# Kernel optimization log

Hardware: AMD Instinct MI355X
Metric: run time of the kernel (lower is better)

## Reference

```python
import jax, jax.numpy as jnp
import numpy as np

B, C, N, K = 32, 1024, 2048, 64


def fps_indices(x, num):
    """Farthest-feature sampling. x: (B, N, C). Returns int32 indices (B, num).
    Deterministic start at index 0 (standard PointNet++ style loop)."""
    b, n, _ = x.shape

    def step(carry, _):
        dists, farthest = carry
        centroid = jnp.take_along_axis(x, farthest[:, None, None], axis=1)  # (B,1,C)
        d = jnp.sum((x - centroid) ** 2, axis=-1)  # (B,N)
        dists = jnp.minimum(dists, d)
        nxt = jnp.argmax(dists, axis=1).astype(jnp.int32)
        return (dists, nxt), farthest

    init = (jnp.full((b, n), 1e10, x.dtype), jnp.zeros((b,), jnp.int32))
    _, idx = jax.lax.scan(step, init, None, length=num)
    return idx.T  # (B, num)


def conv1x1(w, bias, x):
    # w: (out,in), x: (B,in,n) -> (B,out,n)
    return jnp.einsum('oi,bin->bon', w, x) + bias[:, None]


def setup_inputs() -> dict:
    key = jax.random.key(0)
    ks = jax.random.split(key, 16)
    s = 0.02
    return {
        'point_feat': jax.random.normal(ks[0], (B, C, N), jnp.float32),
        'global_feat': jax.random.normal(ks[1], (B, C), jnp.float32),
        'ps1_w': jax.random.normal(ks[2], (C, 128, K), jnp.float32) * s,
        'ps1_b': jnp.zeros((128,), jnp.float32),
        'm1c1_w': jax.random.normal(ks[3], (128, 2 * C + 128), jnp.float32) * s,
        'm1c1_b': jnp.zeros((128,), jnp.float32),
        'm1c2_w': jax.random.normal(ks[4], (128, 128), jnp.float32) * s,
        'm1c2_b': jnp.zeros((128,), jnp.float32),
        'm1sc_w': jax.random.normal(ks[5], (128, 2 * C + 128), jnp.float32) * s,
        'm1sc_b': jnp.zeros((128,), jnp.float32),
        'm2c1_w': jax.random.normal(ks[6], (64, 128), jnp.float32) * s,
        'm2c1_b': jnp.zeros((64,), jnp.float32),
        'm2c2_w': jax.random.normal(ks[7], (3, 64), jnp.float32) * s,
        'm2c2_b': jnp.zeros((3,), jnp.float32),
    }


def reference(point_feat, global_feat, ps1_w, ps1_b, m1c1_w, m1c1_b,
              m1c2_w, m1c2_b, m1sc_w, m1sc_b, m2c1_w, m2c1_b, m2c2_w, m2c2_b):
    # ffs: farthest-feature sample + gather
    xt = jnp.transpose(point_feat, (0, 2, 1))            # (B,N,C)
    idx = fps_indices(xt, K)                             # (B,K)
    feat_ffs = jnp.take_along_axis(xt, idx[:, :, None], axis=1)  # (B,K,C)
    feat_ffs = jnp.transpose(feat_ffs, (0, 2, 1))        # (B,C,K)

    # ConvTranspose1d on a length-1 input == outer product with kernel
    x1 = jnp.einsum('bi,iok->bok', global_feat, ps1_w) + ps1_b[:, None]  # (B,128,K)

    gf = jnp.broadcast_to(global_feat[:, :, None], (B, C, K))
    cat = jnp.concatenate([x1, feat_ffs, gf], axis=1)    # (B,2176,K)

    # MLP_Res
    shortcut = conv1x1(m1sc_w, m1sc_b, cat)
    h = conv1x1(m1c2_w, m1c2_b, jax.nn.relu(conv1x1(m1c1_w, m1c1_b, cat))) + shortcut

    # mlp_2
    pred = conv1x1(m2c2_w, m2c2_b, jax.nn.relu(conv1x1(m2c1_w, m2c1_b, h)))  # (B,3,K)
    return jnp.transpose(pred, (0, 2, 1))                # (B,K,3)
```

## Files before the change

### kernel.cpp

```cpp
#include <hip/hip_runtime.h>

#define BB_ 32
#define CC_ 1024
#define NN_ 2048
#define KK_ 64

typedef __bf16 bf16x8 __attribute__((ext_vector_type(8)));
typedef __bf16 bf16x2 __attribute__((ext_vector_type(2)));
typedef float f32x4 __attribute__((ext_vector_type(4)));
typedef unsigned int u32;

__device__ inline unsigned short f2bf_rn(float f) {
    unsigned u = __float_as_uint(f);
    unsigned r = (u + 0x7fffu + ((u >> 16) & 1u)) >> 16;
    return (unsigned short)r;
}

__device__ inline unsigned pack_bf16_rn(float f0, float f1) {
#if __has_builtin(__builtin_amdgcn_cvt_pk_bf16_f32)
    union { bf16x2 v; unsigned u; } x;
    x.v = __builtin_amdgcn_cvt_pk_bf16_f32(f0, f1);
    return x.u;
#else
    return (unsigned)f2bf_rn(f0) | ((unsigned)f2bf_rn(f1) << 16);
#endif
}

__device__ inline void gload16(const void* g, void* l) {
    __builtin_amdgcn_global_load_lds(
        (const __attribute__((address_space(1))) u32*)g,
        (__attribute__((address_space(3))) u32*)l, 16, 0, 0);
}

__device__ void convert_body(const float* __restrict__ X,
                             unsigned char* __restrict__ Xc, int g0,
                             int cid, int t) {
    int chunk = cid & 7;
    int kt = (cid >> 3) & 31;
    int lb = cid >> 8;
    int n = chunk * 256 + t;
    int b = g0 + lb;
    const float* Xb = X + (size_t)b * CC_ * NN_;
    unsigned char* dst = Xc + (((size_t)lb * 32 + kt) * NN_ + n) * 128;
    int sw = n & 7;
#pragma unroll
    for (int q = 0; q < 4; q++) {
        float f[8];
#pragma unroll
        for (int j = 0; j < 8; j++)
            f[j] = Xb[(size_t)(kt * 32 + q * 8 + j) * NN_ + n];
        union { unsigned u[4]; uint4 v; } hq, lq;
#pragma unroll
        for (int j2 = 0; j2 < 4; j2++) {
            float a = f[2 * j2], c = f[2 * j2 + 1];
            unsigned hp = pack_bf16_rn(a, c);
            float h0f = __uint_as_float((hp & 0xffffu) << 16);
            float h1f = __uint_as_float(hp & 0xffff0000u);
            hq.u[j2] = hp;
            lq.u[j2] = pack_bf16_rn(a - h0f, c - h1f);
        }
        int p = q ^ sw;
        *(uint4*)(dst + (p << 4)) = hq.v;
        *(uint4*)(dst + ((p ^ 4) << 4)) = lq.v;
    }
}

__global__ void convert_kernel(const float* __restrict__ X,
                               unsigned char* __restrict__ Xc, int g0) {
    convert_body(X, Xc, g0, blockIdx.x, threadIdx.x);
}

__device__ void fps_block(const float* Gb, int* idx, int b) {
    __shared__ float swv[2][4];
    __shared__ int swi[2][4];
    int t = threadIdx.x;
    float dist[8], nr[8];
#pragma unroll
    for (int r = 0; r < 8; r++) {
        nr[r] = Gb[(size_t)(t + 256 * r) * (NN_ + 1)];
        dist[r] = 1e10f;
    }
    if (t == 0) idx[b * KK_] = 0;
    int far = 0;
    for (int k = 1; k < KK_; k++) {
        float nf = Gb[(size_t)far * (NN_ + 1)];
        const float* grow = Gb + (size_t)far * NN_;
        float v = -1.f;
        int pi = 0;
#pragma unroll
        for (int r = 0; r < 8; r++) {
            float d = nr[r] + nf - 2.f * grow[t + 256 * r];
            dist[r] = fminf(dist[r], d);
            if (dist[r] > v) { v = dist[r]; pi = t + 256 * r; }
        }
#pragma unroll
        for (int off = 32; off; off >>= 1) {
            float ov = __shfl_down(v, off);
            int oi = __shfl_down(pi, off);
            if (ov > v || (ov == v && oi < pi)) { v = ov; pi = oi; }
        }
        int par = k & 1;
        if ((t & 63) == 0) { swv[par][t >> 6] = v; swi[par][t >> 6] = pi; }
        __syncthreads();
        float bv = swv[par][0];
        int bi = swi[par][0];
#pragma unroll
        for (int ww = 1; ww < 4; ww++) {
            float wv2 = swv[par][ww]; int wi2 = swi[par][ww];
            if (wv2 > bv || (wv2 == bv && wi2 < bi)) { bv = wv2; bi = wi2; }
        }
        far = bi;
        if (t == 0) idx[b * KK_ + k] = bi;
    }
}

__global__ __launch_bounds__(256, 3) void gram_fps_kernel(
    const unsigned char* __restrict__ Xc, float* __restrict__ G,
    const float* Gprev, int* __restrict__ idx, int nFps, int g0prev,
    const float* __restrict__ X, unsigned char* __restrict__ XcNext,
    int g0next, int nGram, int gs) {
    int bx = (int)blockIdx.x;
    if (bx < nFps) {
        fps_block(Gprev + (size_t)bx * NN_ * NN_, idx, g0prev + bx);
        return;
    }
    bx -= nFps;
    if (bx >= nGram) {
        convert_body(X, XcNext, g0next, bx - nGram, threadIdx.x);
        return;
    }
    int lb = bx % gs;
    int tt = bx / gs;
    int tn = (int)((sqrtf(8.f * tt + 1.f) - 1.f) * 0.5f);
    while ((tn + 1) * (tn + 2) / 2 <= tt) tn++;
    while (tn * (tn + 1) / 2 > tt) tn--;
    int tm = tt - tn * (tn + 1) / 2;
    bool diag = (tm == tn);
    int t = threadIdx.x;
    __shared__ __align__(16) unsigned char sA[16384];
    __shared__ __align__(16) unsigned char sB[16384];

    const unsigned char* XcB = Xc + (size_t)lb * 32 * NN_ * 128;
    int w = t >> 6, l = t & 63;
    int m0w = (w & 1) * 64, n0w = (w >> 1) * 64;
    int q = l >> 4, rr = l & 15;

    f32x4 zero = {0.f, 0.f, 0.f, 0.f};
    f32x4 acc[4][4];
#pragma unroll
    for (int mt = 0; mt < 4; mt++)
#pragma unroll
        for (int nt = 0; nt < 4; nt++) acc[mt][nt] = zero;

    const unsigned char* sBp = diag ? sA : sB;
    for (int kt = 0; kt < 32; kt++) {
        const unsigned char* Ab = XcB + ((size_t)kt * NN_ + (size_t)tm * 128) * 128;
        const unsigned char* Bb = XcB + ((size_t)kt * NN_ + (size_t)tn * 128) * 128;
        __syncthreads();
#pragma unroll
        for (int r = 0; r < 4; r++)
            gload16(Ab + r * 4096 + t * 16, sA + r * 4096 + t * 16);
        if (!diag) {
#pragma unroll
            for (int r = 0; r < 4; r++)
                gload16(Bb + r * 4096 + t * 16, sB + r * 4096 + t * 16);
        }
        __syncthreads();

        bf16x8 ah[4], al[4], bh[4], bl[4];
#pragma unroll
        for (int mt = 0; mt < 4; mt++) {
            int ra = m0w + mt * 16 + rr;
            int pa = q ^ (ra & 7);
            ah[mt] = *(const bf16x8*)(sA + ra * 128 + (pa << 4));
            al[mt] = *(const bf16x8*)(sA + ra * 128 + ((pa ^ 4) << 4));
            int rb = n0w + mt * 16 + rr;
            int pb = q ^ (rb & 7);
            bh[mt] = *(const bf16x8*)(sBp + rb * 128 + (pb << 4));
            bl[mt] = *(const bf16x8*)(sBp + rb * 128 + ((pb ^ 4) << 4));
        }
#pragma unroll
        for (int mt = 0; mt < 4; mt++)
#pragma unroll
            for (int nt = 0; nt < 4; nt++) {
                acc[mt][nt] = __builtin_amdgcn_mfma_f32_16x16x32_bf16(ah[mt], bh[nt], acc[mt][nt], 0, 0, 0);
                acc[mt][nt] = __builtin_amdgcn_mfma_f32_16x16x32_bf16(ah[mt], bl[nt], acc[mt][nt], 0, 0, 0);
                acc[mt][nt] = __builtin_amdgcn_mfma_f32_16x16x32_bf16(al[mt], bh[nt], acc[mt][nt], 0, 0, 0);
            }
    }

    float* Gb = G + (size_t)lb * NN_ * NN_;
    int i0 = tm * 128, j0 = tn * 128;
    int cc = l & 15;
#pragma unroll
    for (int mt = 0; mt < 4; mt++)
#pragma unroll
        for (int nt = 0; nt < 4; nt++)
#pragma unroll
            for (int r = 0; r < 4; r++) {
                int gi = i0 + m0w + mt * 16 + q * 4 + r;
                int gj = j0 + n0w + nt * 16 + cc;
                float val = acc[mt][nt][r];
                Gb[(size_t)gi * NN_ + gj] = val;
                if (!diag) Gb[(size_t)gj * NN_ + gi] = val;
            }
}

__global__ void x1_fps_kernel(const float* __restrict__ gf, const float* __restrict__ w,
                              const float* __restrict__ bias, float* __restrict__ cat,
                              const float* Gprev, int* __restrict__ idx,
                              int g0prev, int nFps) {
    if ((int)blockIdx.x < nFps) {
        fps_block(Gprev + (size_t)blockIdx.x * NN_ * NN_, idx, g0prev + blockIdx.x);
        return;
    }
    int bid = blockIdx.x - nFps;
    int t = threadIdx.x;
    int okg = bid & 31, bg = bid >> 5;
    int ok = okg * 256 + t;
    int o = ok >> 6, k = ok & 63;
    float acc[8];
#pragma unroll
    for (int j = 0; j < 8; j++) acc[j] = 0.f;
    const float* g = gf + (size_t)(bg * 8) * CC_;
    for (int i = 0; i < CC_; i++) {
        float wv = w[(size_t)(i * 128 + o) * KK_ + k];
#pragma unroll
        for (int j = 0; j < 8; j++) acc[j] += g[j * CC_ + i] * wv;
    }
    float bv = bias[o];
#pragma unroll
    for (int j = 0; j < 8; j++)
        cat[((size_t)(bg * 8 + j) * 2176 + o) * KK_ + k] = acc[j] + bv;
}

__global__ void catfill_kernel(const float* __restrict__ X, const float* __restrict__ gf,
                               const int* __restrict__ idx, float* __restrict__ cat) {
    int b = blockIdx.y;
    int t = threadIdx.x;
    int ch = 128 + blockIdx.x * 4 + (t >> 6);
    int k = t & 63;
    float v;
    if (ch < 1152) {
        int c = ch - 128;
        int ik = idx[b * KK_ + k];
        v = X[((size_t)b * CC_ + c) * NN_ + ik];
    } else {
        v = gf[b * CC_ + (ch - 1152)];
    }
    cat[((size_t)b * 2176 + ch) * KK_ + k] = v;
}

__global__ void mlp1_kernel(const float* __restrict__ cat, const float* __restrict__ w1,
                            const float* __restrict__ b1, const float* __restrict__ wsc,
                            const float* __restrict__ bsc, float* __restrict__ t1,
                            float* __restrict__ sc) {
    __shared__ float red[2][16][64];
    int b = blockIdx.y, og = blockIdx.x;
    int t = threadIdx.x;
    int k = t & 63, sub = t >> 6;
    int o0 = og * 4;
    const float* cb = cat + (size_t)b * 2176 * KK_;
    float a1[4], a2[4];
#pragma unroll
    for (int j = 0; j < 4; j++) { a1[j] = 0.f; a2[j] = 0.f; }
    int iBeg = sub * 544;
    int off = (b & 7) * 68;
#pragma unroll 1
    for (int seg = 0; seg < 2; seg++) {
        int s0 = iBeg + (seg ? 0 : off);
        int s1 = seg ? iBeg + off : iBeg + 544;
        for (int i = s0; i < s1; i += 4) {
            float v0 = cb[(i + 0) * KK_ + k];
            float v1 = cb[(i + 1) * KK_ + k];
            float v2 = cb[(i + 2) * KK_ + k];
            float v3 = cb[(i + 3) * KK_ + k];
#pragma unroll
            for (int j = 0; j < 4; j++) {
                float4 wv = *(const float4*)(w1 + (size_t)(o0 + j) * 2176 + i);
                a1[j] += wv.x * v0 + wv.y * v1 + wv.z * v2 + wv.w * v3;
                float4 ws = *(const float4*)(wsc + (size_t)(o0 + j) * 2176 + i);
                a2[j] += ws.x * v0 + ws.y * v1 + ws.z * v2 + ws.w * v3;
            }
        }
    }
#pragma unroll
    for (int j = 0; j < 4; j++) {
        red[0][sub * 4 + j][k] = a1[j];
        red[1][sub * 4 + j][k] = a2[j];
    }
    __syncthreads();
#pragma unroll
    for (int p = t; p < 512; p += 256) {
        int m = p >> 8;
        int j = (p >> 6) & 3;
        int kk = p & 63;
        float s = red[m][j][kk] + red[m][4 + j][kk] + red[m][8 + j][kk] + red[m][12 + j][kk];
        int o = o0 + j;
        size_t oidx = ((size_t)b * 128 + o) * KK_ + kk;
        if (m == 0) t1[oidx] = fmaxf(s + b1[o], 0.f);
        else        sc[oidx] = s + bsc[o];
    }
}

__global__ void mlp2_kernel(const float* __restrict__ t1, const float* __restrict__ sc,
                            const float* __restrict__ w2, const float* __restrict__ b2,
                            const float* __restrict__ w3, const float* __restrict__ b3,
                            const float* __restrict__ w4, const float* __restrict__ b4,
                            float* __restrict__ out) {
    __shared__ float sT[128 * 64];
    __shared__ float sH[128 * 64];
    __shared__ float sR[64 * 64];
    int b = blockIdx.x, t = threadIdx.x;
    const float4* t1b4 = (const float4*)(t1 + (size_t)b * 8192);
    for (int j = t; j < 2048; j += 256) ((float4*)sT)[j] = t1b4[j];
    __syncthreads();
    int k = t & 63, og = t >> 6;
    const float* scb = sc + (size_t)b * 8192;

#pragma unroll
    for (int pass = 0; pass < 4; pass++) {
        int o0 = og * 32 + pass * 8;
        float acc[8];
#pragma unroll
        for (int j = 0; j < 8; j++) acc[j] = b2[o0 + j] + scb[(o0 + j) * 64 + k];
        for (int i4 = 0; i4 < 32; i4++) {
            float v0 = sT[(i4 * 4 + 0) * 64 + k];
            float v1 = sT[(i4 * 4 + 1) * 64 + k];
            float v2 = sT[(i4 * 4 + 2) * 64 + k];
            float v3 = sT[(i4 * 4 + 3) * 64 + k];
#pragma unroll
            for (int j = 0; j < 8; j++) {
                float4 wv = *(const float4*)(w2 + (size_t)(o0 + j) * 128 + i4 * 4);
                acc[j] += wv.x * v0 + wv.y * v1 + wv.z * v2 + wv.w * v3;
            }
        }
#pragma unroll
        for (int j = 0; j < 8; j++) sH[(o0 + j) * 64 + k] = acc[j];
    }
    __syncthreads();

#pragma unroll
    for (int pass = 0; pass < 2; pass++) {
        int o0 = og * 16 + pass * 8;
        float acc[8];
#pragma unroll
        for (int j = 0; j < 8; j++) acc[j] = b3[o0 + j];
        for (int i4 = 0; i4 < 32; i4++) {
            float v0 = sH[(i4 * 4 + 0) * 64 + k];
            float v1 = sH[(i4 * 4 + 1) * 64 + k];
            float v2 = sH[(i4 * 4 + 2) * 64 + k];
            float v3 = sH[(i4 * 4 + 3) * 64 + k];
#pragma unroll
            for (int j = 0; j < 8; j++) {
                float4 wv = *(const float4*)(w3 + (size_t)(o0 + j) * 128 + i4 * 4);
                acc[j] += wv.x * v0 + wv.y * v1 + wv.z * v2 + wv.w * v3;
            }
        }
#pragma unroll
        for (int j = 0; j < 8; j++) sR[(o0 + j) * 64 + k] = fmaxf(acc[j], 0.f);
    }
    __syncthreads();

    if (t < 192) {
        int o = t % 3;
        int kk = t / 3;
        float a0 = 0.f, a1 = 0.f, a2 = 0.f, a3 = 0.f;
        for (int i4 = 0; i4 < 16; i4++) {
            float4 wv = *(const float4*)(w4 + o * 64 + i4 * 4);
            a0 += wv.x * sR[(i4 * 4 + 0) * 64 + kk];
            a1 += wv.y * sR[(i4 * 4 + 1) * 64 + kk];
            a2 += wv.z * sR[(i4 * 4 + 2) * 64 + kk];
            a3 += wv.w * sR[(i4 * 4 + 3) * 64 + kk];
        }
        out[((size_t)b * KK_ + kk) * 3 + o] = b4[o] + ((a0 + a1) + (a2 + a3));
    }
}

extern "C" void kernel_launch(void* const* d_in, const int* in_sizes, int n_in,
                              void* d_out, int out_size, void* d_ws, size_t ws_size,
                              hipStream_t stream) {
    const float* X    = (const float*)d_in[0];
    const float* gf   = (const float*)d_in[1];
    const float* ps1w = (const float*)d_in[2];
    const float* ps1b = (const float*)d_in[3];
    const float* w1   = (const float*)d_in[4];
    const float* b1   = (const float*)d_in[5];
    const float* w2   = (const float*)d_in[6];
    const float* b2   = (const float*)d_in[7];
    const float* wsc  = (const float*)d_in[8];
    const float* bscp = (const float*)d_in[9];
    const float* w3   = (const float*)d_in[10];
    const float* b3   = (const float*)d_in[11];
    const float* w4   = (const float*)d_in[12];
    const float* b4   = (const float*)d_in[13];
    float* out = (float*)d_out;

    const size_t G_PER  = (size_t)NN_ * NN_ * 4;
    const size_t XC_PER = (size_t)32 * NN_ * 128;
    const size_t IDX_B  = (size_t)BB_ * KK_ * 4;
    const size_t CAT_B  = (size_t)BB_ * 2176 * KK_ * 4;
    const size_t T1_B   = (size_t)BB_ * 128 * KK_ * 4;
    size_t rest = IDX_B + CAT_B + 2 * T1_B;

    int gs = 1, merged = 0, pipe = 0;
    {
        const int tg[8]  = {8, 8, 4, 4, 2, 2, 1, 1};
        const int tmg[8] = {1, 1, 1, 1, 1, 1, 1, 0};
        const int tp[8]  = {1, 0, 1, 0, 1, 0, 0, 0};
        for (int i = 0; i < 8; i++) {
            size_t need = (size_t)(tmg[i] ? 2 : 1) * tg[i] * G_PER
                        + (size_t)(tp[i] ? 2 : 1) * tg[i] * XC_PER + rest;
            if (ws_size >= need) { gs = tg[i]; merged = tmg[i]; pipe = tp[i]; break; }
        }
    }

    char* ws = (char*)d_ws;
    float* Gbuf = (float*)ws;
    size_t gBufBytes = (size_t)(merged ? 2 : 1) * gs * G_PER;
    unsigned char* Xc0 = (unsigned char*)(ws + gBufBytes);
    unsigned char* Xc1 = Xc0 + (pipe ? (size_t)gs * XC_PER : 0);
    char* p = (char*)Xc0 + (size_t)(pipe ? 2 : 1) * gs * XC_PER;
    int* idxws = (int*)p;    p += IDX_B;
    float* cat = (float*)p;  p += CAT_B;
    float* t1  = (float*)p;  p += T1_B;
    float* sc  = (float*)p;

    int ng = BB_ / gs;
    size_t halfElems = (size_t)gs * NN_ * NN_;
    int nGram = gs * 136;
    int nConvAll = 256 * gs;

    if (pipe) convert_kernel<<<nConvAll, 256, 0, stream>>>(X, Xc0, 0);
    for (int g = 0; g < ng; g++) {
        int g0 = g * gs;
        unsigned char* Xcur  = (g & 1) ? Xc1 : Xc0;
        unsigned char* Xnext = (g & 1) ? Xc0 : Xc1;
        if (!pipe) {
            Xcur = Xc0;
            convert_kernel<<<nConvAll, 256, 0, stream>>>(X, Xc0, g0);
        }
        float* Gcur = Gbuf + (merged ? (size_t)(g & 1) * halfElems : 0);
        float* Gprev = Gbuf + (merged ? (size_t)((g & 1) ^ 1) * halfElems : 0);
        int nFps = (merged && g > 0) ? gs : 0;
        int nConv = (pipe && g < ng - 1) ? nConvAll : 0;
        gram_fps_kernel<<<nFps + nGram + nConv, 256, 0, stream>>>(
            Xcur, Gcur, Gprev, idxws, nFps, g0 - gs, X, Xnext, g0 + gs, nGram, gs);
        if (!merged) {
            gram_fps_kernel<<<gs, 256, 0, stream>>>(
                Xcur, Gcur, Gcur, idxws, gs, g0, X, Xnext, 0, 0, gs);
        }
    }
    int nFpsLast = merged ? gs : 0;
    float* Glast = Gbuf + (merged ? (size_t)((ng - 1) & 1) * halfElems : 0);
    x1_fps_kernel<<<nFpsLast + 128, 256, 0, stream>>>(
        gf, ps1w, ps1b, cat, Glast, idxws, BB_ - gs, nFpsLast);
    catfill_kernel<<<dim3(512, BB_), 256, 0, stream>>>(X, gf, idxws, cat);
    mlp1_kernel<<<dim3(32, BB_), 256, 0, stream>>>(cat, w1, b1, wsc, bscp, t1, sc);
    mlp2_kernel<<<BB_, 256, 0, stream>>>(t1, sc, w2, b2, w3, b3, w4, b4, out);
}
```

Before: 1.374 ms.

## Double-buffer Gram tile loads and stage transposed write through LDS

Result: faster. 1.306 ms (-4.9%).

```diff
diff --git a/kernel.cpp b/kernel.cpp
--- a/kernel.cpp
+++ b/kernel.cpp
@@ -114,7 +114,7 @@
     }
 }
 
-__global__ __launch_bounds__(256, 3) void gram_fps_kernel(
+__global__ __launch_bounds__(256, 2) void gram_fps_kernel(
     const unsigned char* __restrict__ Xc, float* __restrict__ G,
     const float* Gprev, int* __restrict__ idx, int nFps, int g0prev,
     const float* __restrict__ X, unsigned char* __restrict__ XcNext,
@@ -137,8 +137,7 @@
     int tm = tt - tn * (tn + 1) / 2;
     bool diag = (tm == tn);
     int t = threadIdx.x;
-    __shared__ __align__(16) unsigned char sA[16384];
-    __shared__ __align__(16) unsigned char sB[16384];
+    __shared__ __align__(16) unsigned char sMem[128 * 132 * 4];
 
     const unsigned char* XcB = Xc + (size_t)lb * 32 * NN_ * 128;
     int w = t >> 6, l = t & 63;
@@ -152,32 +151,43 @@
 #pragma unroll
         for (int nt = 0; nt < 4; nt++) acc[mt][nt] = zero;
 
-    const unsigned char* sBp = diag ? sA : sB;
-    for (int kt = 0; kt < 32; kt++) {
+    auto stage = [&](int buf, int kt) {
         const unsigned char* Ab = XcB + ((size_t)kt * NN_ + (size_t)tm * 128) * 128;
         const unsigned char* Bb = XcB + ((size_t)kt * NN_ + (size_t)tn * 128) * 128;
-        __syncthreads();
-#pragma unroll
-        for (int r = 0; r < 4; r++)
-            gload16(Ab + r * 4096 + t * 16, sA + r * 4096 + t * 16);
-        if (!diag) {
-#pragma unroll
-            for (int r = 0; r < 4; r++)
-                gload16(Bb + r * 4096 + t * 16, sB + r * 4096 + t * 16);
-        }
-        __syncthreads();
-
+        unsigned char* dA = sMem + buf * 32768;
+        unsigned char* dB = dA + 16384;
+#pragma unroll
+        for (int r = 0; r < 4; r++) {
+            gload16(Ab + r * 4096 + t * 16, dA + r * 4096 + t * 16);
+            gload16(Bb + r * 4096 + t * 16, dB + r * 4096 + t * 16);
+        }
+    };
+
+    stage(0, 0);
+    for (int kt = 0; kt < 32; kt++) {
+        int c = kt & 1;
+        if (kt < 31) {
+            stage(c ^ 1, kt + 1);
+            asm volatile("s_waitcnt vmcnt(8)" ::: "memory");
+        } else {
+            asm volatile("s_waitcnt vmcnt(0)" ::: "memory");
+        }
+        __builtin_amdgcn_sched_barrier(0);
+        __builtin_amdgcn_s_barrier();
+
+        const unsigned char* cA = sMem + c * 32768;
+        const unsigned char* cB = cA + 16384;
         bf16x8 ah[4], al[4], bh[4], bl[4];
 #pragma unroll
         for (int mt = 0; mt < 4; mt++) {
             int ra = m0w + mt * 16 + rr;
             int pa = q ^ (ra & 7);
-            ah[mt] = *(const bf16x8*)(sA + ra * 128 + (pa << 4));
-            al[mt] = *(const bf16x8*)(sA + ra * 128 + ((pa ^ 4) << 4));
+            ah[mt] = *(const bf16x8*)(cA + ra * 128 + (pa << 4));
+            al[mt] = *(const bf16x8*)(cA + ra * 128 + ((pa ^ 4) << 4));
             int rb = n0w + mt * 16 + rr;
             int pb = q ^ (rb & 7);
-            bh[mt] = *(const bf16x8*)(sBp + rb * 128 + (pb << 4));
-            bl[mt] = *(const bf16x8*)(sBp + rb * 128 + ((pb ^ 4) << 4));
+            bh[mt] = *(const bf16x8*)(cB + rb * 128 + (pb << 4));
+            bl[mt] = *(const bf16x8*)(cB + rb * 128 + ((pb ^ 4) << 4));
         }
 #pragma unroll
         for (int mt = 0; mt < 4; mt++)
@@ -187,23 +197,35 @@
                 acc[mt][nt] = __builtin_amdgcn_mfma_f32_16x16x32_bf16(ah[mt], bl[nt], acc[mt][nt], 0, 0, 0);
                 acc[mt][nt] = __builtin_amdgcn_mfma_f32_16x16x32_bf16(al[mt], bh[nt], acc[mt][nt], 0, 0, 0);
             }
+        __builtin_amdgcn_s_barrier();
     }
 
     float* Gb = G + (size_t)lb * NN_ * NN_;
     int i0 = tm * 128, j0 = tn * 128;
     int cc = l & 15;
+    float* tb = (float*)sMem;
 #pragma unroll
     for (int mt = 0; mt < 4; mt++)
 #pragma unroll
         for (int nt = 0; nt < 4; nt++)
 #pragma unroll
             for (int r = 0; r < 4; r++) {
-                int gi = i0 + m0w + mt * 16 + q * 4 + r;
-                int gj = j0 + n0w + nt * 16 + cc;
+                int gi = m0w + mt * 16 + q * 4 + r;
+                int gj = n0w + nt * 16 + cc;
                 float val = acc[mt][nt][r];
-                Gb[(size_t)gi * NN_ + gj] = val;
-                if (!diag) Gb[(size_t)gj * NN_ + gi] = val;
+                Gb[(size_t)(i0 + gi) * NN_ + j0 + gj] = val;
+                if (!diag) tb[gj * 132 + gi] = val;
             }
+    if (!diag) {
+        __syncthreads();
+#pragma unroll
+        for (int m = 0; m < 16; m++) {
+            int f = t + 256 * m;
+            int jj = f >> 5, sg = f & 31;
+            float4 v4 = *(const float4*)(tb + jj * 132 + sg * 4);
+            *(float4*)(&Gb[(size_t)(j0 + jj) * NN_ + i0 + sg * 4]) = v4;
+        }
+    }
 }
 
 __global__ void x1_fps_kernel(const float* __restrict__ gf, const float* __restrict__ w,
```
